# Kernel tuning notes

Hardware: AMD Instinct MI355X
Metric: run time of the kernel (lower is better)

The kernel has to match this reference:

```python
import jax, jax.numpy as jnp
import numpy as np

B, T, IN, H, OUT = 128, 1024, 128, 256, 4


def _uniform(key, shape, k):
    return jax.random.uniform(key, shape, jnp.float32, -k, k)


def setup_inputs() -> dict:
    key = jax.random.key(0)
    ks = jax.random.split(key, 20)
    k = 1.0 / np.sqrt(H)
    inp = {"data": jax.random.normal(ks[0], (B, T, IN), jnp.float32)}
    # layer 0: per-direction stacked weights, PyTorch gate order (r, z, n)
    inp["w_ih_l0"] = _uniform(ks[1], (2, 3 * H, IN), k)
    inp["w_hh_l0"] = _uniform(ks[2], (2, 3 * H, H), k)
    inp["b_ih_l0"] = _uniform(ks[3], (2, 3 * H), k)
    inp["b_hh_l0"] = _uniform(ks[4], (2, 3 * H), k)
    # layer 1: input is concat of both directions -> 2H
    inp["w_ih_l1"] = _uniform(ks[5], (2, 3 * H, 2 * H), k)
    inp["w_hh_l1"] = _uniform(ks[6], (2, 3 * H, H), k)
    inp["b_ih_l1"] = _uniform(ks[7], (2, 3 * H), k)
    inp["b_hh_l1"] = _uniform(ks[8], (2, 3 * H), k)
    # output head: Linear(2H -> OUT)
    ko = 1.0 / np.sqrt(2 * H)
    inp["w_out"] = _uniform(ks[9], (OUT, 2 * H), ko)
    inp["b_out"] = _uniform(ks[10], (OUT,), ko)
    return inp


def _gru_direction(x, w_ih, w_hh, b_ih, b_hh, reverse):
    """Single-direction GRU over x [B, T, D]. Returns (outputs [B,T,H], h_last [B,H])."""
    bsz = x.shape[0]
    # precompute input projections for all timesteps: [T, B, 3H]
    px = jnp.einsum('btd,gd->tbg', x, w_ih) + b_ih

    def step(h, px_t):
        ph = h @ w_hh.T + b_hh                     # [B, 3H]
        xr, xz, xn = jnp.split(px_t, 3, axis=-1)
        hr, hz, hn = jnp.split(ph, 3, axis=-1)
        r = jax.nn.sigmoid(xr + hr)
        z = jax.nn.sigmoid(xz + hz)
        n = jnp.tanh(xn + r * hn)
        h_new = (1.0 - z) * n + z * h
        return h_new, h_new

    h0 = jnp.zeros((bsz, w_hh.shape[1]), x.dtype)
    h_last, ys = jax.lax.scan(step, h0, px, reverse=reverse)
    return jnp.swapaxes(ys, 0, 1), h_last          # [B, T, H], [B, H]


def _bigru_layer(x, w_ih, w_hh, b_ih, b_hh):
    """Bidirectional GRU layer; params stacked [2, ...] (fwd, bwd)."""
    yf, hf = _gru_direction(x, w_ih[0], w_hh[0], b_ih[0], b_hh[0], reverse=False)
    yb, hb = _gru_direction(x, w_ih[1], w_hh[1], b_ih[1], b_hh[1], reverse=True)
    return jnp.concatenate([yf, yb], axis=-1), hf, hb


def reference(data, w_ih_l0, w_hh_l0, b_ih_l0, b_hh_l0,
              w_ih_l1, w_hh_l1, b_ih_l1, b_hh_l1, w_out, b_out):
    y0, _, _ = _bigru_layer(data, w_ih_l0, w_hh_l0, b_ih_l0, b_hh_l0)
    # inter-layer dropout is identity in eval mode
    _, hf, hb = _bigru_layer(y0, w_ih_l1, w_hh_l1, b_ih_l1, b_hh_l1)
    hidden = jnp.concatenate([hf, hb], axis=1)     # [B, 2H] (final dropout = eval identity)
    return hidden @ w_out.T + b_out                # [B, OUT]
```

## Files before the change

### kernel.cpp

```cpp
#include <hip/hip_runtime.h>


typedef _Float16 f16;
typedef __attribute__((ext_vector_type(8))) _Float16 f16x8;
typedef __attribute__((ext_vector_type(4))) _Float16 f16x4;
typedef __attribute__((ext_vector_type(4))) float f32x4;

constexpr int BB  = 128;
constexpr int TT  = 1024;
constexpr int INF = 128;
constexpr int HH  = 256;
constexpr int G3  = 768;
constexpr int DD2 = 512;
constexpr int TC  = 128;
constexpr int NCH = TT / TC;
constexpr int SLAB = 16 * G3;

constexpr float SR = -1.44269504f;
constexpr float SN = 2.88539009f;

#define MF(a, b, c) __builtin_amdgcn_mfma_f32_16x16x32_f16(a, b, c, 0, 0, 0)

__global__ void convw(const float* __restrict__ a, const float* __restrict__ b,
                      const float* __restrict__ c, const float* __restrict__ d,
                      f16* __restrict__ oa, f16* __restrict__ ob,
                      f16* __restrict__ oc, f16* __restrict__ od) {
  int i = blockIdx.x * blockDim.x + threadIdx.x;
  int s = gridDim.x * blockDim.x;
  for (int j = i; j < 2 * G3 * INF; j += s) oa[j] = (f16)a[j];
  for (int j = i; j < 2 * G3 * HH;  j += s) ob[j] = (f16)b[j];
  for (int j = i; j < 2 * G3 * DD2; j += s) oc[j] = (f16)c[j];
  for (int j = i; j < 2 * G3 * HH;  j += s) od[j] = (f16)d[j];
}

template <int KD, bool AF16>
__global__ __launch_bounds__(256) void px_gemm(const void* __restrict__ Ain,
                                               const f16* __restrict__ W,
                                               const float* __restrict__ bih,
                                               const float* __restrict__ bhh,
                                               f16* __restrict__ px, int c) {
  __shared__ __align__(16) f16 As[128][40];
  __shared__ __align__(16) f16 Bs[64][40];
  const int d = blockIdx.z, mt = blockIdx.x, nt = blockIdx.y;
  const int t = d ? (TT - 1 - (c * TC + mt)) : (c * TC + mt);
  const int tid = threadIdx.x, lane = tid & 63, w = tid >> 6;
  const int wm = w >> 1, wn = w & 1;
  const f16* Wd = W + (size_t)d * G3 * KD;
  f32x4 acc[4][2];
  const f32x4 zz = {0.f, 0.f, 0.f, 0.f};
#pragma unroll
  for (int mi = 0; mi < 4; ++mi)
#pragma unroll
    for (int ni = 0; ni < 2; ++ni) acc[mi][ni] = zz;

  for (int kb = 0; kb < KD / 32; ++kb) {
    const int k0 = kb * 32;
    if constexpr (AF16) {
      const f16* A = (const f16*)Ain;
#pragma unroll
      for (int p = 0; p < 2; ++p) {
        int idx = p * 256 + tid;
        int row = idx >> 2, kc = idx & 3;
        f16x8 v = *(const f16x8*)(A + ((size_t)t * BB + row) * DD2 + k0 + kc * 8);
        *(f16x8*)&As[row][kc * 8] = v;
      }
    } else {
      const float* A = (const float*)Ain;
#pragma unroll
      for (int p = 0; p < 4; ++p) {
        int idx = p * 256 + tid;
        int row = idx >> 3, kc = idx & 7;
        const float* srcp = A + (size_t)row * (TT * INF) + t * INF + k0 + kc * 4;
        float4 v = *(const float4*)srcp;
        f16x4 h4;
        h4[0] = (f16)v.x; h4[1] = (f16)v.y; h4[2] = (f16)v.z; h4[3] = (f16)v.w;
        *(f16x4*)&As[row][kc * 4] = h4;
      }
    }
    {
      int row = tid >> 2, kc = tid & 3;
      f16x8 v = *(const f16x8*)(Wd + (size_t)(nt * 64 + row) * KD + k0 + kc * 8);
      *(f16x8*)&Bs[row][kc * 8] = v;
    }
    __syncthreads();
#pragma unroll
    for (int mi = 0; mi < 4; ++mi) {
      f16x8 av = *(const f16x8*)&As[wm * 64 + mi * 16 + (lane & 15)][(lane >> 4) * 8];
#pragma unroll
      for (int ni = 0; ni < 2; ++ni) {
        f16x8 bv = *(const f16x8*)&Bs[wn * 32 + ni * 16 + (lane & 15)][(lane >> 4) * 8];
        acc[mi][ni] = __builtin_amdgcn_mfma_f32_16x16x32_f16(av, bv, acc[mi][ni], 0, 0, 0);
      }
    }
    __syncthreads();
  }

  float bias[2], scale[2];
#pragma unroll
  for (int ni = 0; ni < 2; ++ni) {
    int col = nt * 64 + wn * 32 + ni * 16 + (lane & 15);
    if (col < 2 * HH) { scale[ni] = SR; bias[ni] = bih[d * G3 + col] + bhh[d * G3 + col]; }
    else              { scale[ni] = SN; bias[ni] = bih[d * G3 + col]; }
  }
#pragma unroll
  for (int mi = 0; mi < 4; ++mi)
#pragma unroll
    for (int ni = 0; ni < 2; ++ni)
#pragma unroll
      for (int r = 0; r < 4; ++r) {
        int brow = wm * 64 + mi * 16 + (lane >> 4) * 4 + r;
        int col = nt * 64 + wn * 32 + ni * 16 + (lane & 15);
        int g = col >> 8, ch = col & 255;
        size_t slab = (size_t)((d * TC + mt) * 8 + (brow >> 4)) * SLAB;
        int off = ((ch >> 5) * 64 + ((brow & 15) >> 2) * 16 + (ch & 15)) * 24 +
                  (g * 2 + ((ch >> 4) & 1)) * 4 + (brow & 3);
        px[slab + off] = (f16)(scale[ni] * (acc[mi][ni][r] + bias[ni]));
      }
}

template <int LAYER>
__global__ __launch_bounds__(512, 2) void recur(const f16* __restrict__ px,
                                                const f16* __restrict__ whh,
                                                const float* __restrict__ bhh,
                                                float* __restrict__ hstate,
                                                f16* __restrict__ y0, int c) {
  __shared__ __align__(16) f16 hbuf[2 * 16 * 256];
  char* HB = (char*)hbuf;
  const int d = blockIdx.x >> 3, b0 = (blockIdx.x & 7) * 16;
  const int tid = threadIdx.x, lane = tid & 63, w = tid >> 6;
  const int cl = lane & 15, hi = lane >> 4, r0 = hi * 4;

  const f16* wd = whh + (size_t)d * G3 * HH;
  f16x8 bf[3][2][8];
#pragma unroll
  for (int g = 0; g < 3; ++g)
#pragma unroll
    for (int ct = 0; ct < 2; ++ct)
#pragma unroll
      for (int kt = 0; kt < 8; ++kt) {
        int col = g * HH + w * 32 + ct * 16 + cl;
        int k = kt * 32 + hi * 8;
        bf[g][ct][kt] = *(const f16x8*)(wd + (size_t)col * HH + k);
      }
  float bn[2];
#pragma unroll
  for (int ct = 0; ct < 2; ++ct)
    bn[ct] = bhh[d * G3 + 2 * HH + w * 32 + ct * 16 + cl];

  const unsigned vb = cl * 512 + ((hi * 16) ^ ((cl & 3) << 4));
  const unsigned wbase = hi * 4 * 512 + w * 64 + (cl & 7) * 2 + (((cl >> 3) & 1) << 4);
  const unsigned wb0 = wbase, wb1 = wbase ^ 16;

  float hreg[2][4];
  if (c == 0) {
#pragma unroll
    for (int ct = 0; ct < 2; ++ct)
#pragma unroll
      for (int r = 0; r < 4; ++r) hreg[ct][r] = 0.f;
    for (int j = tid; j < 16 * 256; j += 512) hbuf[j] = (f16)0.f;
  } else {
#pragma unroll
    for (int ct = 0; ct < 2; ++ct)
#pragma unroll
      for (int r = 0; r < 4; ++r) {
        float v = hstate[((size_t)d * BB + b0 + r0 + r) * HH + w * 32 + ct * 16 + cl];
        hreg[ct][r] = v;
        unsigned wa = ((r & 1) ? wb1 : wb0) + r * 512 + ((ct ^ ((r >> 1) & 1)) << 5);
        *(f16*)(HB + wa) = (f16)v;
      }
  }

  const f16* pp = px + (size_t)(d * TC * 8 + (b0 >> 4)) * SLAB + (size_t)(w * 64 + lane) * 24;
  f16* ypt = nullptr;
  ptrdiff_t ystep = 0;
  if constexpr (LAYER == 0) {
    int t0 = d ? (TT - 1 - c * TC) : (c * TC);
    ypt = y0 + ((size_t)t0 * BB + b0 + hi * 4) * DD2 + d * HH + w * 32 + cl;
    ystep = d ? -(ptrdiff_t)(BB * DD2) : (ptrdiff_t)(BB * DD2);
  }

  for (int ib = 0; ib < TC; ib += 2) {
#pragma unroll
    for (int s = 0; s < 2; ++s) {
      const int roB = s ? 8192 : 0;
      const int wrB = s ? 0 : 8192;
      asm volatile("s_waitcnt lgkmcnt(0)" ::: "memory");
      __builtin_amdgcn_sched_barrier(0);
      __builtin_amdgcn_s_barrier();
      __builtin_amdgcn_sched_barrier(0);

      f16x8 p0 = *(const f16x8*)(pp);
      f16x8 p1 = *(const f16x8*)(pp + 8);
      f16x8 p2 = *(const f16x8*)(pp + 16);
      pp += 8 * SLAB;

      f32x4 acc[3][2];
      const f32x4 zz = {0.f, 0.f, 0.f, 0.f};
#pragma unroll
      for (int ct = 0; ct < 2; ++ct) {
        acc[0][ct] = zz;
        acc[1][ct] = zz;
        acc[2][ct] = (f32x4){bn[ct], bn[ct], bn[ct], bn[ct]};
      }

      f16x8 a0 = *(const f16x8*)(HB + vb + roB + 0 * 64);
      f16x8 a1 = *(const f16x8*)(HB + vb + roB + 1 * 64);
      f16x8 a2 = *(const f16x8*)(HB + vb + roB + 2 * 64);
#pragma unroll
      for (int kt = 0; kt < 8; ++kt) {
        f16x8 an;
        if (kt < 5) an = *(const f16x8*)(HB + vb + roB + (kt + 3) * 64);
        acc[0][0] = MF(a0, bf[0][0][kt], acc[0][0]);
        acc[0][1] = MF(a0, bf[0][1][kt], acc[0][1]);
        acc[1][0] = MF(a0, bf[1][0][kt], acc[1][0]);
        acc[1][1] = MF(a0, bf[1][1][kt], acc[1][1]);
        acc[2][0] = MF(a0, bf[2][0][kt], acc[2][0]);
        acc[2][1] = MF(a0, bf[2][1][kt], acc[2][1]);
        a0 = a1; a1 = a2; a2 = an;
      }

#pragma unroll
      for (int ct = 0; ct < 2; ++ct)
#pragma unroll
        for (int r = 0; r < 4; ++r) {
          float pr = (float)p0[ct * 4 + r];
          float pz = (float)p1[ct * 4 + r];
          float pn = (float)p2[ct * 4 + r];
          float er = __builtin_amdgcn_exp2f(__builtin_fmaf(acc[0][ct][r], SR, pr));
          float rg = __builtin_amdgcn_rcpf(1.f + er);
          float ez = __builtin_amdgcn_exp2f(__builtin_fmaf(acc[1][ct][r], SR, pz));
          float zg = __builtin_amdgcn_rcpf(1.f + ez);
          float en = __builtin_amdgcn_exp2f(__builtin_fmaf(rg * SN, acc[2][ct][r], pn));
          float tn = __builtin_amdgcn_rcpf(1.f + en);
          float ng = __builtin_fmaf(-2.f, tn, 1.f);
          float hv = __builtin_fmaf(zg, hreg[ct][r] - ng, ng);
          hreg[ct][r] = hv;
          unsigned wa = ((r & 1) ? wb1 : wb0) + r * 512 + ((ct ^ ((r >> 1) & 1)) << 5) + wrB;
          *(f16*)(HB + wa) = (f16)hv;
          if constexpr (LAYER == 0) ypt[r * DD2 + ct * 16] = (f16)hv;
        }
      if constexpr (LAYER == 0) ypt += ystep;
    }
  }
#pragma unroll
  for (int ct = 0; ct < 2; ++ct)
#pragma unroll
    for (int r = 0; r < 4; ++r)
      hstate[((size_t)d * BB + b0 + r0 + r) * HH + w * 32 + ct * 16 + cl] = hreg[ct][r];
}

__global__ void head(const float* __restrict__ hstate, const float* __restrict__ wout,
                     const float* __restrict__ bout, float* __restrict__ out) {
  int g = blockIdx.x * blockDim.x + threadIdx.x;
  if (g >= BB * 4) return;
  int b = g >> 2, o = g & 3;
  float s = bout[o];
  for (int jj = 0; jj < DD2; ++jj) {
    int dd = jj >> 8, j = jj & 255;
    s += hstate[((size_t)dd * BB + b) * HH + j] * wout[o * DD2 + jj];
  }
  out[g] = s;
}

extern "C" void kernel_launch(void* const* d_in, const int* in_sizes, int n_in,
                              void* d_out, int out_size, void* d_ws, size_t ws_size,
                              hipStream_t stream) {
  const float* data = (const float*)d_in[0];
  const float* wih0 = (const float*)d_in[1];
  const float* whh0 = (const float*)d_in[2];
  const float* bih0 = (const float*)d_in[3];
  const float* bhh0 = (const float*)d_in[4];
  const float* wih1 = (const float*)d_in[5];
  const float* whh1 = (const float*)d_in[6];
  const float* bih1 = (const float*)d_in[7];
  const float* bhh1 = (const float*)d_in[8];
  const float* wout = (const float*)d_in[9];
  const float* bout = (const float*)d_in[10];

  char* ws = (char*)d_ws;
  f16*   f_wih0 = (f16*)(ws + 0);
  f16*   f_whh0 = (f16*)(ws + 393216);
  f16*   f_wih1 = (f16*)(ws + 1179648);
  f16*   f_whh1 = (f16*)(ws + 2752512);
  float* hstate = (float*)(ws + 3538944);
  f16*   y0     = (f16*)(ws + 4194304);
  f16*   px     = (f16*)(ws + 138412032);

  convw<<<512, 256, 0, stream>>>(wih0, whh0, wih1, whh1, f_wih0, f_whh0, f_wih1, f_whh1);

  dim3 gg(TC, 12, 2);
  for (int c = 0; c < NCH; ++c) {
    px_gemm<INF, false><<<gg, 256, 0, stream>>>(data, f_wih0, bih0, bhh0, px, c);
    recur<0><<<16, 512, 0, stream>>>(px, f_whh0, bhh0, hstate, y0, c);
  }
  for (int c = 0; c < NCH; ++c) {
    px_gemm<DD2, true><<<gg, 256, 0, stream>>>(y0, f_wih1, bih1, bhh1, px, c);
    recur<1><<<16, 512, 0, stream>>>(px, f_whh1, bhh1, hstate, nullptr, c);
  }
  head<<<4, 128, 0, stream>>>(hstate, wout, bout, (float*)d_out);
}
```

Before: 4.352 ms.

## Fuse next-chunk input projection GEMM into recurrence kernel with double-buffered px

Merges the per-chunk input-projection GEMM and the GRU recurrence into one kernel launch. The first 16 blocks run the sequential recurrence for chunk c while the remaining blocks compute projections for chunk c+1 into a second px buffer, so the GEMM overlaps the latency-bound recurrence instead of running serially before it. The chunk size is halved, which doubles the number of launches, and the LDS swizzle for the hidden-state buffer is changed. Sharing CUs between GEMM blocks and recurrence blocks may slow the critical-path recurrence.

```diff
diff --git a/kernel.cpp b/kernel.cpp
--- a/kernel.cpp
+++ b/kernel.cpp
@@ -12,9 +12,11 @@
 constexpr int HH  = 256;
 constexpr int G3  = 768;
 constexpr int DD2 = 512;
-constexpr int TC  = 128;
+constexpr int TC  = 64;
 constexpr int NCH = TT / TC;
 constexpr int SLAB = 16 * G3;
+constexpr int PXCHUNK = 2 * TC * 8 * SLAB;
+constexpr int NPXB = TC * 6 * 2;
 
 constexpr float SR = -1.44269504f;
 constexpr float SN = 2.88539009f;
@@ -33,220 +35,226 @@
   for (int j = i; j < 2 * G3 * HH;  j += s) od[j] = (f16)d[j];
 }
 
-template <int KD, bool AF16>
-__global__ __launch_bounds__(256) void px_gemm(const void* __restrict__ Ain,
-                                               const f16* __restrict__ W,
-                                               const float* __restrict__ bih,
-                                               const float* __restrict__ bhh,
-                                               f16* __restrict__ px, int c) {
-  __shared__ __align__(16) f16 As[128][40];
-  __shared__ __align__(16) f16 Bs[64][40];
-  const int d = blockIdx.z, mt = blockIdx.x, nt = blockIdx.y;
-  const int t = d ? (TT - 1 - (c * TC + mt)) : (c * TC + mt);
+template <int LAYER, int PXKD, bool PXF16, bool HASRECUR>
+__global__ __launch_bounds__(512, 2) void fused(
+    const f16* __restrict__ pxin, f16* __restrict__ pxout,
+    const f16* __restrict__ whh, const float* __restrict__ bhh,
+    float* __restrict__ hstate, f16* __restrict__ y0,
+    const void* __restrict__ pxA, const f16* __restrict__ wih,
+    const float* __restrict__ bih, const float* __restrict__ bhhpx,
+    int c, int cpx) {
+  __shared__ __align__(16) char smem[20480];
   const int tid = threadIdx.x, lane = tid & 63, w = tid >> 6;
-  const int wm = w >> 1, wn = w & 1;
-  const f16* Wd = W + (size_t)d * G3 * KD;
-  f32x4 acc[4][2];
-  const f32x4 zz = {0.f, 0.f, 0.f, 0.f};
-#pragma unroll
-  for (int mi = 0; mi < 4; ++mi)
-#pragma unroll
-    for (int ni = 0; ni < 2; ++ni) acc[mi][ni] = zz;
-
-  for (int kb = 0; kb < KD / 32; ++kb) {
-    const int k0 = kb * 32;
-    if constexpr (AF16) {
-      const f16* A = (const f16*)Ain;
-#pragma unroll
-      for (int p = 0; p < 2; ++p) {
-        int idx = p * 256 + tid;
-        int row = idx >> 2, kc = idx & 3;
-        f16x8 v = *(const f16x8*)(A + ((size_t)t * BB + row) * DD2 + k0 + kc * 8);
-        *(f16x8*)&As[row][kc * 8] = v;
+  const int cl = lane & 15, hi = lane >> 4;
+
+  if (HASRECUR && blockIdx.x < 16) {
+    char* HB = smem;
+    const int bid = blockIdx.x;
+    const int d = bid >> 3, b0 = (bid & 7) * 16, r0 = hi * 4;
+
+    const f16* wd = whh + (size_t)d * G3 * HH;
+    f16x8 bf[3][2][8];
+#pragma unroll
+    for (int g = 0; g < 3; ++g)
+#pragma unroll
+      for (int ct = 0; ct < 2; ++ct)
+#pragma unroll
+        for (int kt = 0; kt < 8; ++kt) {
+          int col = g * HH + w * 32 + ct * 16 + cl;
+          int k = kt * 32 + hi * 8;
+          bf[g][ct][kt] = *(const f16x8*)(wd + (size_t)col * HH + k);
+        }
+    float bn[2];
+#pragma unroll
+    for (int ct = 0; ct < 2; ++ct)
+      bn[ct] = bhh[d * G3 + 2 * HH + w * 32 + ct * 16 + cl];
+
+    const unsigned rb = (unsigned)cl * 512 + (((unsigned)hi * 16) ^ ((unsigned)(cl & 3) << 4)) +
+                        ((unsigned)(cl & 4) << 4);
+    unsigned wbase[4];
+#pragma unroll
+    for (int r = 0; r < 4; ++r)
+      wbase[r] = (unsigned)(hi * 4 + r) * 512 +
+                 ((((unsigned)w * 64) + (unsigned)cl * 2) ^
+                  ((((unsigned)hi & 1) << 6) | ((unsigned)r << 4))) +
+                 ((r & 2) ? -32 : 0);
+
+    float hreg[2][4];
+    if (c == 0) {
+#pragma unroll
+      for (int ct = 0; ct < 2; ++ct)
+#pragma unroll
+        for (int r = 0; r < 4; ++r) hreg[ct][r] = 0.f;
+      for (int j = tid; j < 16 * 256; j += 512) ((f16*)HB)[j] = (f16)0.f;
+    } else {
+#pragma unroll
+      for (int ct = 0; ct < 2; ++ct)
+#pragma unroll
+        for (int r = 0; r < 4; ++r) {
+          int row = r0 + r, col = w * 32 + ct * 16 + cl;
+          float v = hstate[((size_t)d * BB + b0 + row) * HH + col];
+          hreg[ct][r] = v;
+          unsigned wa = (unsigned)row * 512 + (((unsigned)col * 2) ^ ((unsigned)(row & 7) << 4));
+          *(f16*)(HB + wa) = (f16)v;
+        }
+    }
+
+    const f16* pp = pxin + (size_t)(d * TC * 8 + (bid & 7)) * SLAB + (size_t)(w * 64 + lane) * 24;
+    f16* ypt = nullptr;
+    ptrdiff_t ystep = 0;
+    if constexpr (LAYER == 0) {
+      int t0 = d ? (TT - 1 - c * TC) : (c * TC);
+      ypt = y0 + ((size_t)t0 * BB + b0 + hi * 4) * DD2 + d * HH + w * 32 + cl;
+      ystep = d ? -(ptrdiff_t)(BB * DD2) : (ptrdiff_t)(BB * DD2);
+    }
+
+    for (int ib = 0; ib < TC; ib += 2) {
+#pragma unroll
+      for (int s = 0; s < 2; ++s) {
+        const int roB = s ? 8192 : 0;
+        const int wrB = s ? 0 : 8192;
+        asm volatile("s_waitcnt lgkmcnt(0)" ::: "memory");
+        __builtin_amdgcn_sched_barrier(0);
+        __builtin_amdgcn_s_barrier();
+        __builtin_amdgcn_sched_barrier(0);
+
+        f16x8 p0 = *(const f16x8*)(pp);
+        f16x8 p1 = *(const f16x8*)(pp + 8);
+        f16x8 p2 = *(const f16x8*)(pp + 16);
+        pp += 8 * SLAB;
+
+        f32x4 acc[3][2];
+        const f32x4 zz = {0.f, 0.f, 0.f, 0.f};
+#pragma unroll
+        for (int ct = 0; ct < 2; ++ct) {
+          acc[0][ct] = zz;
+          acc[1][ct] = zz;
+          acc[2][ct] = (f32x4){bn[ct], bn[ct], bn[ct], bn[ct]};
+        }
+
+        f16x8 a0 = *(const f16x8*)(HB + ((rb ^ (0u << 6)) + roB));
+        f16x8 a1 = *(const f16x8*)(HB + ((rb ^ (1u << 6)) + roB));
+        f16x8 a2 = *(const f16x8*)(HB + ((rb ^ (2u << 6)) + roB));
+#pragma unroll
+        for (int kt = 0; kt < 8; ++kt) {
+          f16x8 an;
+          if (kt < 5) an = *(const f16x8*)(HB + ((rb ^ ((unsigned)(kt + 3) << 6)) + roB));
+          acc[0][0] = MF(a0, bf[0][0][kt], acc[0][0]);
+          acc[0][1] = MF(a0, bf[0][1][kt], acc[0][1]);
+          acc[1][0] = MF(a0, bf[1][0][kt], acc[1][0]);
+          acc[1][1] = MF(a0, bf[1][1][kt], acc[1][1]);
+          acc[2][0] = MF(a0, bf[2][0][kt], acc[2][0]);
+          acc[2][1] = MF(a0, bf[2][1][kt], acc[2][1]);
+          a0 = a1; a1 = a2; a2 = an;
+        }
+
+#pragma unroll
+        for (int ct = 0; ct < 2; ++ct)
+#pragma unroll
+          for (int r = 0; r < 4; ++r) {
+            float pr = (float)p0[ct * 4 + r];
+            float pz = (float)p1[ct * 4 + r];
+            float pn = (float)p2[ct * 4 + r];
+            float er = __builtin_amdgcn_exp2f(__builtin_fmaf(acc[0][ct][r], SR, pr));
+            float rg = __builtin_amdgcn_rcpf(1.f + er);
+            float ez = __builtin_amdgcn_exp2f(__builtin_fmaf(acc[1][ct][r], SR, pz));
+            float zg = __builtin_amdgcn_rcpf(1.f + ez);
+            float en = __builtin_amdgcn_exp2f(__builtin_fmaf(rg * SN, acc[2][ct][r], pn));
+            float tn = __builtin_amdgcn_rcpf(1.f + en);
+            float ng = __builtin_fmaf(-2.f, tn, 1.f);
+            float hv = __builtin_fmaf(zg, hreg[ct][r] - ng, ng);
+            hreg[ct][r] = hv;
+            unsigned wa = wbase[r] + (ct ? ((r & 2) ? 0 : 32) : ((r & 2) ? 32 : 0)) + wrB;
+            *(f16*)(HB + wa) = (f16)hv;
+            if constexpr (LAYER == 0) ypt[r * DD2 + ct * 16] = (f16)hv;
+          }
+        if constexpr (LAYER == 0) ypt += ystep;
       }
-    } else {
-      const float* A = (const float*)Ain;
-#pragma unroll
-      for (int p = 0; p < 4; ++p) {
-        int idx = p * 256 + tid;
-        int row = idx >> 3, kc = idx & 7;
-        const float* srcp = A + (size_t)row * (TT * INF) + t * INF + k0 + kc * 4;
-        float4 v = *(const float4*)srcp;
-        f16x4 h4;
-        h4[0] = (f16)v.x; h4[1] = (f16)v.y; h4[2] = (f16)v.z; h4[3] = (f16)v.w;
-        *(f16x4*)&As[row][kc * 4] = h4;
+    }
+#pragma unroll
+    for (int ct = 0; ct < 2; ++ct)
+#pragma unroll
+      for (int r = 0; r < 4; ++r)
+        hstate[((size_t)d * BB + b0 + r0 + r) * HH + w * 32 + ct * 16 + cl] = hreg[ct][r];
+    return;
+  }
+
+  {
+    const int pb = HASRECUR ? (int)blockIdx.x - 16 : (int)blockIdx.x;
+    const int mt = pb & (TC - 1), rest = pb >> 6;
+    const int pair = rest % 6, d = rest / 6;
+    const int t = d ? (TT - 1 - (cpx * TC + mt)) : (cpx * TC + mt);
+    f16 (*As)[40] = (f16(*)[40])smem;
+    f16* Bsf = (f16*)(smem + 10240);
+    const int wn = w & 1, wm = (w >> 1) & 1, ntsub = w >> 2;
+    const int nt = pair * 2 + ntsub;
+    const f16* Wd = wih + (size_t)d * G3 * PXKD;
+
+    f32x4 acc[4][2];
+    const f32x4 zz = {0.f, 0.f, 0.f, 0.f};
+#pragma unroll
+    for (int mi = 0; mi < 4; ++mi)
+#pragma unroll
+      for (int ni = 0; ni < 2; ++ni) acc[mi][ni] = zz;
+
+    for (int kb = 0; kb < PXKD / 32; ++kb) {
+      const int k0 = kb * 32;
+      {
+        int row = tid >> 2, kc = tid & 3;
+        if constexpr (PXF16) {
+          const f16* A = (const f16*)pxA;
+          f16x8 v = *(const f16x8*)(A + ((size_t)t * BB + row) * DD2 + k0 + kc * 8);
+          *(f16x8*)&As[row][kc * 8] = v;
+        } else {
+          const float* A = (const float*)pxA;
+#pragma unroll
+          for (int p = 0; p < 2; ++p) {
+            float4 v = *(const float4*)(A + (size_t)row * (TT * INF) + t * INF + k0 + kc * 8 + p * 4);
+            f16x4 h4;
+            h4[0] = (f16)v.x; h4[1] = (f16)v.y; h4[2] = (f16)v.z; h4[3] = (f16)v.w;
+            *(f16x4*)&As[row][kc * 8 + p * 4] = h4;
+          }
+        }
+        int nts = tid >> 8, t2 = tid & 255;
+        int brow = t2 >> 2, bkc = t2 & 3;
+        f16x8 v = *(const f16x8*)(Wd + (size_t)((pair * 2 + nts) * 64 + brow) * PXKD + k0 + bkc * 8);
+        *(f16x8*)&Bsf[(nts * 64 + brow) * 40 + bkc * 8] = v;
       }
-    }
-    {
-      int row = tid >> 2, kc = tid & 3;
-      f16x8 v = *(const f16x8*)(Wd + (size_t)(nt * 64 + row) * KD + k0 + kc * 8);
-      *(f16x8*)&Bs[row][kc * 8] = v;
-    }
-    __syncthreads();
-#pragma unroll
-    for (int mi = 0; mi < 4; ++mi) {
-      f16x8 av = *(const f16x8*)&As[wm * 64 + mi * 16 + (lane & 15)][(lane >> 4) * 8];
-#pragma unroll
-      for (int ni = 0; ni < 2; ++ni) {
-        f16x8 bv = *(const f16x8*)&Bs[wn * 32 + ni * 16 + (lane & 15)][(lane >> 4) * 8];
-        acc[mi][ni] = __builtin_amdgcn_mfma_f32_16x16x32_f16(av, bv, acc[mi][ni], 0, 0, 0);
+      __syncthreads();
+#pragma unroll
+      for (int mi = 0; mi < 4; ++mi) {
+        f16x8 av = *(const f16x8*)&As[wm * 64 + mi * 16 + cl][hi * 8];
+#pragma unroll
+        for (int ni = 0; ni < 2; ++ni) {
+          f16x8 bv = *(const f16x8*)&Bsf[(ntsub * 64 + wn * 32 + ni * 16 + cl) * 40 + hi * 8];
+          acc[mi][ni] = __builtin_amdgcn_mfma_f32_16x16x32_f16(av, bv, acc[mi][ni], 0, 0, 0);
+        }
       }
-    }
-    __syncthreads();
-  }
-
-  float bias[2], scale[2];
-#pragma unroll
-  for (int ni = 0; ni < 2; ++ni) {
-    int col = nt * 64 + wn * 32 + ni * 16 + (lane & 15);
-    if (col < 2 * HH) { scale[ni] = SR; bias[ni] = bih[d * G3 + col] + bhh[d * G3 + col]; }
-    else              { scale[ni] = SN; bias[ni] = bih[d * G3 + col]; }
-  }
-#pragma unroll
-  for (int mi = 0; mi < 4; ++mi)
-#pragma unroll
-    for (int ni = 0; ni < 2; ++ni)
-#pragma unroll
-      for (int r = 0; r < 4; ++r) {
-        int brow = wm * 64 + mi * 16 + (lane >> 4) * 4 + r;
-        int col = nt * 64 + wn * 32 + ni * 16 + (lane & 15);
-        int g = col >> 8, ch = col & 255;
-        size_t slab = (size_t)((d * TC + mt) * 8 + (brow >> 4)) * SLAB;
-        int off = ((ch >> 5) * 64 + ((brow & 15) >> 2) * 16 + (ch & 15)) * 24 +
-                  (g * 2 + ((ch >> 4) & 1)) * 4 + (brow & 3);
-        px[slab + off] = (f16)(scale[ni] * (acc[mi][ni][r] + bias[ni]));
-      }
-}
-
-template <int LAYER>
-__global__ __launch_bounds__(512, 2) void recur(const f16* __restrict__ px,
-                                                const f16* __restrict__ whh,
-                                                const float* __restrict__ bhh,
-                                                float* __restrict__ hstate,
-                                                f16* __restrict__ y0, int c) {
-  __shared__ __align__(16) f16 hbuf[2 * 16 * 256];
-  char* HB = (char*)hbuf;
-  const int d = blockIdx.x >> 3, b0 = (blockIdx.x & 7) * 16;
-  const int tid = threadIdx.x, lane = tid & 63, w = tid >> 6;
-  const int cl = lane & 15, hi = lane >> 4, r0 = hi * 4;
-
-  const f16* wd = whh + (size_t)d * G3 * HH;
-  f16x8 bf[3][2][8];
-#pragma unroll
-  for (int g = 0; g < 3; ++g)
-#pragma unroll
-    for (int ct = 0; ct < 2; ++ct)
-#pragma unroll
-      for (int kt = 0; kt < 8; ++kt) {
-        int col = g * HH + w * 32 + ct * 16 + cl;
-        int k = kt * 32 + hi * 8;
-        bf[g][ct][kt] = *(const f16x8*)(wd + (size_t)col * HH + k);
-      }
-  float bn[2];
-#pragma unroll
-  for (int ct = 0; ct < 2; ++ct)
-    bn[ct] = bhh[d * G3 + 2 * HH + w * 32 + ct * 16 + cl];
-
-  const unsigned vb = cl * 512 + ((hi * 16) ^ ((cl & 3) << 4));
-  const unsigned wbase = hi * 4 * 512 + w * 64 + (cl & 7) * 2 + (((cl >> 3) & 1) << 4);
-  const unsigned wb0 = wbase, wb1 = wbase ^ 16;
-
-  float hreg[2][4];
-  if (c == 0) {
-#pragma unroll
-    for (int ct = 0; ct < 2; ++ct)
-#pragma unroll
-      for (int r = 0; r < 4; ++r) hreg[ct][r] = 0.f;
-    for (int j = tid; j < 16 * 256; j += 512) hbuf[j] = (f16)0.f;
-  } else {
-#pragma unroll
-    for (int ct = 0; ct < 2; ++ct)
-#pragma unroll
-      for (int r = 0; r < 4; ++r) {
-        float v = hstate[((size_t)d * BB + b0 + r0 + r) * HH + w * 32 + ct * 16 + cl];
-        hreg[ct][r] = v;
-        unsigned wa = ((r & 1) ? wb1 : wb0) + r * 512 + ((ct ^ ((r >> 1) & 1)) << 5);
-        *(f16*)(HB + wa) = (f16)v;
-      }
-  }
-
-  const f16* pp = px + (size_t)(d * TC * 8 + (b0 >> 4)) * SLAB + (size_t)(w * 64 + lane) * 24;
-  f16* ypt = nullptr;
-  ptrdiff_t ystep = 0;
-  if constexpr (LAYER == 0) {
-    int t0 = d ? (TT - 1 - c * TC) : (c * TC);
-    ypt = y0 + ((size_t)t0 * BB + b0 + hi * 4) * DD2 + d * HH + w * 32 + cl;
-    ystep = d ? -(ptrdiff_t)(BB * DD2) : (ptrdiff_t)(BB * DD2);
-  }
-
-  for (int ib = 0; ib < TC; ib += 2) {
-#pragma unroll
-    for (int s = 0; s < 2; ++s) {
-      const int roB = s ? 8192 : 0;
-      const int wrB = s ? 0 : 8192;
-      asm volatile("s_waitcnt lgkmcnt(0)" ::: "memory");
-      __builtin_amdgcn_sched_barrier(0);
-      __builtin_amdgcn_s_barrier();
-      __builtin_amdgcn_sched_barrier(0);
-
-      f16x8 p0 = *(const f16x8*)(pp);
-      f16x8 p1 = *(const f16x8*)(pp + 8);
-      f16x8 p2 = *(const f16x8*)(pp + 16);
-      pp += 8 * SLAB;
-
-      f32x4 acc[3][2];
-      const f32x4 zz = {0.f, 0.f, 0.f, 0.f};
-#pragma unroll
-      for (int ct = 0; ct < 2; ++ct) {
-        acc[0][ct] = zz;
-        acc[1][ct] = zz;
-        acc[2][ct] = (f32x4){bn[ct], bn[ct], bn[ct], bn[ct]};
-      }
-
-      f16x8 a0 = *(const f16x8*)(HB + vb + roB + 0 * 64);
-      f16x8 a1 = *(const f16x8*)(HB + vb + roB + 1 * 64);
-      f16x8 a2 = *(const f16x8*)(HB + vb + roB + 2 * 64);
-#pragma unroll
-      for (int kt = 0; kt < 8; ++kt) {
-        f16x8 an;
-        if (kt < 5) an = *(const f16x8*)(HB + vb + roB + (kt + 3) * 64);
-        acc[0][0] = MF(a0, bf[0][0][kt], acc[0][0]);
-        acc[0][1] = MF(a0, bf[0][1][kt], acc[0][1]);
-        acc[1][0] = MF(a0, bf[1][0][kt], acc[1][0]);
-        acc[1][1] = MF(a0, bf[1][1][kt], acc[1][1]);
-        acc[2][0] = MF(a0, bf[2][0][kt], acc[2][0]);
-        acc[2][1] = MF(a0, bf[2][1][kt], acc[2][1]);
-        a0 = a1; a1 = a2; a2 = an;
-      }
-
-#pragma unroll
-      for (int ct = 0; ct < 2; ++ct)
+      __syncthreads();
+    }
+
+    float bias[2], scale[2];
+#pragma unroll
+    for (int ni = 0; ni < 2; ++ni) {
+      int col = nt * 64 + wn * 32 + ni * 16 + cl;
+      if (col < 2 * HH) { scale[ni] = SR; bias[ni] = bih[d * G3 + col] + bhhpx[d * G3 + col]; }
+      else              { scale[ni] = SN; bias[ni] = bih[d * G3 + col]; }
+    }
+#pragma unroll
+    for (int mi = 0; mi < 4; ++mi)
+#pragma unroll
+      for (int ni = 0; ni < 2; ++ni)
 #pragma unroll
         for (int r = 0; r < 4; ++r) {
-          float pr = (float)p0[ct * 4 + r];
-          float pz = (float)p1[ct * 4 + r];
-          float pn = (float)p2[ct * 4 + r];
-          float er = __builtin_amdgcn_exp2f(__builtin_fmaf(acc[0][ct][r], SR, pr));
-          float rg = __builtin_amdgcn_rcpf(1.f + er);
-          float ez = __builtin_amdgcn_exp2f(__builtin_fmaf(acc[1][ct][r], SR, pz));
-          float zg = __builtin_amdgcn_rcpf(1.f + ez);
-          float en = __builtin_amdgcn_exp2f(__builtin_fmaf(rg * SN, acc[2][ct][r], pn));
-          float tn = __builtin_amdgcn_rcpf(1.f + en);
-          float ng = __builtin_fmaf(-2.f, tn, 1.f);
-          float hv = __builtin_fmaf(zg, hreg[ct][r] - ng, ng);
-          hreg[ct][r] = hv;
-          unsigned wa = ((r & 1) ? wb1 : wb0) + r * 512 + ((ct ^ ((r >> 1) & 1)) << 5) + wrB;
-          *(f16*)(HB + wa) = (f16)hv;
-          if constexpr (LAYER == 0) ypt[r * DD2 + ct * 16] = (f16)hv;
-        }
-      if constexpr (LAYER == 0) ypt += ystep;
-    }
-  }
-#pragma unroll
-  for (int ct = 0; ct < 2; ++ct)
-#pragma unroll
-    for (int r = 0; r < 4; ++r)
-      hstate[((size_t)d * BB + b0 + r0 + r) * HH + w * 32 + ct * 16 + cl] = hreg[ct][r];
+          int brow = wm * 64 + mi * 16 + hi * 4 + r;
+          int col = nt * 64 + wn * 32 + ni * 16 + cl;
+          int g = col >> 8, ch = col & 255;
+          size_t slab = (size_t)((d * TC + mt) * 8 + (brow >> 4)) * SLAB;
+          int off = ((ch >> 5) * 64 + ((brow & 15) >> 2) * 16 + (ch & 15)) * 24 +
+                    (g * 2 + ((ch >> 4) & 1)) * 4 + (brow & 3);
+          pxout[slab + off] = (f16)(scale[ni] * (acc[mi][ni][r] + bias[ni]));
+        }
+  }
 }
 
 __global__ void head(const float* __restrict__ hstate, const float* __restrict__ wout,
@@ -284,18 +292,27 @@
   f16*   f_whh1 = (f16*)(ws + 2752512);
   float* hstate = (float*)(ws + 3538944);
   f16*   y0     = (f16*)(ws + 4194304);
-  f16*   px     = (f16*)(ws + 138412032);
+  f16*   pxr    = (f16*)(ws + 138412032);
+
+  f16* slot[2] = {pxr, pxr + PXCHUNK};
 
   convw<<<512, 256, 0, stream>>>(wih0, whh0, wih1, whh1, f_wih0, f_whh0, f_wih1, f_whh1);
 
-  dim3 gg(TC, 12, 2);
+  fused<0, INF, false, false><<<NPXB, 512, 0, stream>>>(
+      nullptr, slot[0], f_whh0, bhh0, hstate, y0, data, f_wih0, bih0, bhh0, 0, 0);
   for (int c = 0; c < NCH; ++c) {
-    px_gemm<INF, false><<<gg, 256, 0, stream>>>(data, f_wih0, bih0, bhh0, px, c);
-    recur<0><<<16, 512, 0, stream>>>(px, f_whh0, bhh0, hstate, y0, c);
-  }
+    int npx = (c + 1 < NCH) ? NPXB : 0;
+    fused<0, INF, false, true><<<16 + npx, 512, 0, stream>>>(
+        slot[c & 1], slot[(c + 1) & 1], f_whh0, bhh0, hstate, y0,
+        data, f_wih0, bih0, bhh0, c, c + 1);
+  }
+  fused<1, DD2, true, false><<<NPXB, 512, 0, stream>>>(
+      nullptr, slot[0], f_whh1, bhh1, hstate, nullptr, y0, f_wih1, bih1, bhh1, 0, 0);
   for (int c = 0; c < NCH; ++c) {
-    px_gemm<DD2, true><<<gg, 256, 0, stream>>>(y0, f_wih1, bih1, bhh1, px, c);
-    recur<1><<<16, 512, 0, stream>>>(px, f_whh1, bhh1, hstate, nullptr, c);
+    int npx = (c + 1 < NCH) ? NPXB : 0;
+    fused<1, DD2, true, true><<<16 + npx, 512, 0, stream>>>(
+        slot[c & 1], slot[(c + 1) & 1], f_whh1, bhh1, hstate, nullptr,
+        y0, f_wih1, bih1, bhh1, c, c + 1);
   }
   head<<<4, 128, 0, stream>>>(hstate, wout, bout, (float*)d_out);
 }
```

Result: faster. 4.226 ms (-2.9%).
